# Kernel tuning notes

Measured on AMD Instinct MI355X. Metric: run time of the kernel, lower is better.

The kernel has to match this reference:

```python
import jax, jax.numpy as jnp
import numpy as np

TAU = 2.0          # LIF membrane time constant
V_TH = 1.0         # spike threshold (spikingjelly default)
BN_EPS = 1e-5

T, C_IN, C_OUT, L = 16, 512, 512, 4096


def setup_inputs() -> dict:
    key = jax.random.key(0)
    k1, k2 = jax.random.split(key)
    x = jax.random.normal(k1, (T, C_IN, L), dtype=jnp.float32)
    W = jax.random.normal(k2, (C_OUT, C_IN), dtype=jnp.float32) * 0.02
    gamma = jnp.ones((C_OUT,), dtype=jnp.float32)
    beta = jnp.zeros((C_OUT,), dtype=jnp.float32)
    return {"x": x, "W": W, "gamma": gamma, "beta": beta}


def reference(x, W, gamma, beta):
    # 1x1 Conv1d (bias=False): [T, Cin, L] x [Cout, Cin] -> [T, Cout, L]
    y = jnp.einsum("tcl,oc->tol", x, W)

    # BatchNorm1d in training mode: normalize per channel over (T, L)
    mean = jnp.mean(y, axis=(0, 2), keepdims=True)
    var = jnp.mean(jnp.square(y - mean), axis=(0, 2), keepdims=True)  # biased var
    y = (y - mean) * jax.lax.rsqrt(var + BN_EPS)
    y = y * gamma[None, :, None] + beta[None, :, None]

    # Multi-step LIF: v' = v + (x - v)/tau ; spike = H(v' - vth) ; hard reset to 0
    def step(v, x_t):
        v = v + (x_t - v) / TAU
        s = (v >= V_TH).astype(v.dtype)
        v = v * (1.0 - s)  # v_reset = 0
        return v, s

    v0 = jnp.zeros_like(y[0])
    _, spikes = jax.lax.scan(step, v0, y)
    return spikes
```

## Files before the change

### kernel.cpp

```cpp
#include <hip/hip_runtime.h>


#define T_STEPS 16
#define CIN 512
#define COUT 512
#define LDIM 4096
#define NL (COUT * LDIM)

static constexpr size_t NY = (size_t)T_STEPS * NL;

__device__ float g_yf[NY];
__device__ float g_wt[CIN * COUT];
__device__ float g_mr[2 * COUT];
__device__ int   g_bf16;

__device__ __forceinline__ float b2f(unsigned short u) {
    return __uint_as_float(((unsigned int)u) << 16);
}

__global__ void detect_dtype(const unsigned int* __restrict__ gamma_words) {
    if (threadIdx.x == 0)
        g_bf16 = (gamma_words[0] == 0x3F803F80u) ? 1 : 0;
}

__global__ __launch_bounds__(256) void wrepack(const void* __restrict__ win) {
    const int idx = blockIdx.x * 256 + threadIdx.x;
    const int k = idx >> 9;
    const int o = idx & 511;
    float v;
    if (g_bf16) v = b2f(((const unsigned short*)win)[(size_t)o * CIN + k]);
    else        v = ((const float*)win)[(size_t)o * CIN + k];
    g_wt[(size_t)k * COUT + o] = v;
}

__global__ __launch_bounds__(256) void gemm_sg(
    const void* __restrict__ xin, float* __restrict__ yws, int use_ws)
{
#pragma clang fp contract(off)
    float* __restrict__ y = use_ws ? yws : g_yf;
    const int bf = g_bf16;

    const int l  = blockIdx.x * 256 + threadIdx.x;
    const int og = blockIdx.y;
    const int t  = blockIdx.z;

    float acc[32];
    #pragma unroll
    for (int i = 0; i < 32; i++) acc[i] = 0.0f;

    const float* __restrict__ wt = g_wt + og * 32;

    if (bf) {
        const unsigned short* __restrict__ xp =
            (const unsigned short*)xin + (size_t)t * CIN * LDIM + l;
        #pragma unroll 2
        for (int k = 0; k < CIN; k++) {
            const float xv = b2f(xp[(size_t)k * LDIM]);
            const float* __restrict__ wr = wt + (size_t)k * COUT;
            #pragma unroll
            for (int i = 0; i < 32; i++)
                acc[i] = acc[i] + wr[i] * xv;
        }
    } else {
        const float* __restrict__ xp =
            (const float*)xin + (size_t)t * CIN * LDIM + l;
        #pragma unroll 2
        for (int k = 0; k < CIN; k++) {
            const float xv = xp[(size_t)k * LDIM];
            const float* __restrict__ wr = wt + (size_t)k * COUT;
            #pragma unroll
            for (int i = 0; i < 32; i++)
                acc[i] = acc[i] + wr[i] * xv;
        }
    }

    float* __restrict__ yp = y + ((size_t)t * COUT + og * 32) * LDIM + l;
    #pragma unroll
    for (int i = 0; i < 32; i++) yp[(size_t)i * LDIM] = acc[i];
}

__global__ __launch_bounds__(256) void bn_stats_np(
    const float* __restrict__ yws, int use_ws)
{
#pragma clang fp contract(off)
    const float* __restrict__ y = use_ws ? yws : g_yf;
    const int o = blockIdx.x;
    const int g = threadIdx.x >> 3;
    const int l = threadIdx.x & 7;

    __shared__ float leaves[32];
    __shared__ float mean_sh;
    __shared__ float acc_sh[2];

    for (int phase = 0; phase < 2; ++phase) {
        __syncthreads();
        const float mean = (phase == 1) ? mean_sh : 0.0f;
        for (int t = 0; t < T_STEPS; ++t) {
            const float* row = &y[(size_t)t * NL + (size_t)o * LDIM + g * 128];
            float r[8];
            #pragma unroll
            for (int q = 0; q < 8; q++) {
                float a = row[q * 8 + l];
                float b = row[64 + q * 8 + l];
                if (phase == 1) {
                    float da = a - mean; a = da * da;
                    float db = b - mean; b = db * db;
                }
                r[q] = a + b;
            }
            float s01 = r[0] + r[1], s23 = r[2] + r[3];
            float s45 = r[4] + r[5], s67 = r[6] + r[7];
            float S = (s01 + s23) + (s45 + s67);
            S = S + __shfl_xor(S, 1);
            S = S + __shfl_xor(S, 2);
            S = S + __shfl_xor(S, 4);
            __syncthreads();
            if (l == 0) leaves[g] = S;
            __syncthreads();
            if (threadIdx.x == 0) {
                float a16[16], a8[8], a4[4], a2[2];
                #pragma unroll
                for (int k = 0; k < 16; k++) a16[k] = leaves[2*k] + leaves[2*k+1];
                #pragma unroll
                for (int k = 0; k < 8;  k++) a8[k] = a16[2*k] + a16[2*k+1];
                #pragma unroll
                for (int k = 0; k < 4;  k++) a4[k] = a8[2*k] + a8[2*k+1];
                #pragma unroll
                for (int k = 0; k < 2;  k++) a2[k] = a4[2*k] + a4[2*k+1];
                float pw = a2[0] + a2[1];
                if (t == 0) acc_sh[phase] = pw;
                else        acc_sh[phase] = acc_sh[phase] + pw;
            }
            __syncthreads();
        }
        if (threadIdx.x == 0) {
            if (phase == 0) {
                mean_sh = __fdiv_rn(acc_sh[0], 65536.0f);
            } else {
                float var = __fdiv_rn(acc_sh[1], 65536.0f);
                float rr = __fdiv_rn(1.0f, __fsqrt_rn(var + 1e-5f));
                g_mr[o] = mean_sh;
                g_mr[COUT + o] = rr;
            }
        }
    }
}

__global__ __launch_bounds__(256) void lif_np(
    const void* __restrict__ gin, const void* __restrict__ bin,
    void* __restrict__ outv, const float* __restrict__ yws, int use_ws)
{
#pragma clang fp contract(off)
    const float* __restrict__ y = use_ws ? yws : g_yf;
    const int bf = g_bf16;
    const int idx = blockIdx.x * 256 + threadIdx.x;
    const int o = idx >> 12;
    const float mean = g_mr[o];
    const float r    = g_mr[COUT + o];
    float gm, bt;
    if (bf) {
        gm = b2f(((const unsigned short*)gin)[o]);
        bt = b2f(((const unsigned short*)bin)[o]);
    } else {
        gm = ((const float*)gin)[o];
        bt = ((const float*)bin)[o];
    }
    float v = 0.0f;
    #pragma unroll
    for (int t = 0; t < T_STEPS; t++) {
        float yv = y[(size_t)t * NL + idx];
        float d  = yv - mean;
        float n1 = d * r;
        float n2 = n1 * gm;
        float n3 = n2 + bt;
        float dv = n3 - v;
        float h  = dv * 0.5f;
        v = v + h;
        float s;
        if (v >= 1.0f) { s = 1.0f; v = 0.0f; } else { s = 0.0f; }
        if (bf) ((unsigned short*)outv)[(size_t)t * NL + idx] = (s == 1.0f) ? 0x3F80 : 0x0000;
        else    ((float*)outv)[(size_t)t * NL + idx] = s;
    }
}

extern "C" void kernel_launch(void* const* d_in, const int* in_sizes, int n_in,
                              void* d_out, int out_size, void* d_ws, size_t ws_size,
                              hipStream_t stream) {
    const void* x     = d_in[0];
    const void* W     = d_in[1];
    const void* gamma = d_in[2];
    const void* beta  = d_in[3];

    const int use_ws = (ws_size >= NY * sizeof(float)) ? 1 : 0;
    float* yws = (float*)d_ws;

    detect_dtype<<<1, 64, 0, stream>>>((const unsigned int*)gamma);

    wrepack<<<(CIN * COUT) / 256, 256, 0, stream>>>(W);

    dim3 grid(LDIM / 256, COUT / 32, T_STEPS);
    gemm_sg<<<grid, 256, 0, stream>>>(x, yws, use_ws);

    bn_stats_np<<<COUT, 256, 0, stream>>>(yws, use_ws);

    lif_np<<<NL / 256, 256, 0, stream>>>(gamma, beta, d_out, yws, use_ws);
}
```

Baseline: 812.1 us.

## Use packed FP32 mul/add with duplicated weights, two columns per thread

The GEMM now computes two adjacent L columns per thread, using v_pk_mul_f32 and v_pk_add_f32 inline asm. The weight repack stores each weight duplicated into a 64-bit pair so it can be a scalar operand. x loads and y stores become 2-wide vectors, and the grid halves along L. The goal is twice the FP32 throughput per instruction while keeping separate mul and add for bitwise matching. The trade-offs are doubled weight memory, more registers for the accumulators, and half as many threads.

```diff
diff --git a/kernel.cpp b/kernel.cpp
--- a/kernel.cpp
+++ b/kernel.cpp
@@ -6,11 +6,14 @@
 #define COUT 512
 #define LDIM 4096
 #define NL (COUT * LDIM)
+#define LP (LDIM / 2)
 
 static constexpr size_t NY = (size_t)T_STEPS * NL;
 
+typedef float v2f __attribute__((ext_vector_type(2)));
+
 __device__ float g_yf[NY];
-__device__ float g_wt[CIN * COUT];
+__device__ unsigned long long g_wt2[CIN * COUT];
 __device__ float g_mr[2 * COUT];
 __device__ int   g_bf16;
 
@@ -30,53 +33,68 @@
     float v;
     if (g_bf16) v = b2f(((const unsigned short*)win)[(size_t)o * CIN + k]);
     else        v = ((const float*)win)[(size_t)o * CIN + k];
-    g_wt[(size_t)k * COUT + o] = v;
-}
-
-__global__ __launch_bounds__(256) void gemm_sg(
+    const unsigned int b = __float_as_uint(v);
+    g_wt2[(size_t)k * COUT + o] = ((unsigned long long)b << 32) | b;
+}
+
+__global__ __launch_bounds__(256, 4) void gemm_pk(
     const void* __restrict__ xin, float* __restrict__ yws, int use_ws)
 {
 #pragma clang fp contract(off)
     float* __restrict__ y = use_ws ? yws : g_yf;
     const int bf = g_bf16;
 
-    const int l  = blockIdx.x * 256 + threadIdx.x;
+    const int lp = blockIdx.x * 256 + threadIdx.x;
     const int og = blockIdx.y;
     const int t  = blockIdx.z;
 
-    float acc[32];
+    v2f acc[32];
     #pragma unroll
-    for (int i = 0; i < 32; i++) acc[i] = 0.0f;
-
-    const float* __restrict__ wt = g_wt + og * 32;
+    for (int i = 0; i < 32; i++) { acc[i].x = 0.0f; acc[i].y = 0.0f; }
+
+    const unsigned long long* __restrict__ wt = g_wt2 + og * 32;
 
     if (bf) {
-        const unsigned short* __restrict__ xp =
-            (const unsigned short*)xin + (size_t)t * CIN * LDIM + l;
+        const unsigned int* __restrict__ xp =
+            (const unsigned int*)xin + (size_t)t * CIN * LP + lp;
         #pragma unroll 2
         for (int k = 0; k < CIN; k++) {
-            const float xv = b2f(xp[(size_t)k * LDIM]);
-            const float* __restrict__ wr = wt + (size_t)k * COUT;
+            const unsigned int u = xp[(size_t)k * LP];
+            v2f x2;
+            x2.x = __uint_as_float(u << 16);
+            x2.y = __uint_as_float(u & 0xffff0000u);
+            const unsigned long long* __restrict__ wr = wt + (size_t)k * COUT;
             #pragma unroll
-            for (int i = 0; i < 32; i++)
-                acc[i] = acc[i] + wr[i] * xv;
+            for (int i = 0; i < 32; i++) {
+                v2f p;
+                asm("v_pk_mul_f32 %0, %1, %2"
+                    : "=v"(p) : "s"(wr[i]), "v"(x2));
+                asm("v_pk_add_f32 %0, %1, %2"
+                    : "=v"(acc[i]) : "v"(acc[i]), "v"(p));
+            }
         }
     } else {
-        const float* __restrict__ xp =
-            (const float*)xin + (size_t)t * CIN * LDIM + l;
+        const v2f* __restrict__ xp =
+            (const v2f*)xin + (size_t)t * CIN * LP + lp;
         #pragma unroll 2
         for (int k = 0; k < CIN; k++) {
-            const float xv = xp[(size_t)k * LDIM];
-            const float* __restrict__ wr = wt + (size_t)k * COUT;
+            v2f x2 = xp[(size_t)k * LP];
+            const unsigned long long* __restrict__ wr = wt + (size_t)k * COUT;
             #pragma unroll
-            for (int i = 0; i < 32; i++)
-                acc[i] = acc[i] + wr[i] * xv;
-        }
-    }
-
-    float* __restrict__ yp = y + ((size_t)t * COUT + og * 32) * LDIM + l;
+            for (int i = 0; i < 32; i++) {
+                v2f p;
+                asm("v_pk_mul_f32 %0, %1, %2"
+                    : "=v"(p) : "s"(wr[i]), "v"(x2));
+                asm("v_pk_add_f32 %0, %1, %2"
+                    : "=v"(acc[i]) : "v"(acc[i]), "v"(p));
+            }
+        }
+    }
+
+    float* __restrict__ yp = y + ((size_t)t * COUT + og * 32) * LDIM + 2 * lp;
     #pragma unroll
-    for (int i = 0; i < 32; i++) yp[(size_t)i * LDIM] = acc[i];
+    for (int i = 0; i < 32; i++)
+        *(v2f*)(yp + (size_t)i * LDIM) = acc[i];
 }
 
 __global__ __launch_bounds__(256) void bn_stats_np(
@@ -198,8 +216,8 @@
 
     wrepack<<<(CIN * COUT) / 256, 256, 0, stream>>>(W);
 
-    dim3 grid(LDIM / 256, COUT / 32, T_STEPS);
-    gemm_sg<<<grid, 256, 0, stream>>>(x, yws, use_ws);
+    dim3 grid(LDIM / 512, COUT / 32, T_STEPS);
+    gemm_pk<<<grid, 256, 0, stream>>>(x, yws, use_ws);
 
     bn_stats_np<<<COUT, 256, 0, stream>>>(yws, use_ws);
 
```

Result: slower. 829.6 us (+2.2%).

## Rewrite conv GEMM in inline assembly with packed FP32 math and scalar weight loads

Applied to the files above, without the earlier changes.

Replaces the compiler-generated SIMT GEMM with a hand-written assembly loop. Each thread now handles two adjacent L positions, using v_pk_mul/v_pk_add on duplicated weight pairs. The 32 weights per k step are loaded into scalar registers with s_load_dwordx16 instead of per-lane vector loads. A separate pre-pass converts bf16 input to an fp32 buffer so the asm path only handles fp32. The aim is to halve the VALU instruction count and cut redundant weight loads. The cost is a full wait on every k iteration with no prefetch, an extra global fp32 buffer, and fragile hard-coded register clobbers.

```diff
diff --git a/kernel.cpp b/kernel.cpp
--- a/kernel.cpp
+++ b/kernel.cpp
@@ -6,11 +6,14 @@
 #define COUT 512
 #define LDIM 4096
 #define NL (COUT * LDIM)
+#define LP (LDIM / 2)
 
 static constexpr size_t NY = (size_t)T_STEPS * NL;
+static constexpr size_t NX = (size_t)T_STEPS * CIN * LDIM;
 
 __device__ float g_yf[NY];
-__device__ float g_wt[CIN * COUT];
+__device__ float g_xf[NX];
+__device__ unsigned long long g_wt2[CIN * COUT];
 __device__ float g_mr[2 * COUT];
 __device__ int   g_bf16;
 
@@ -30,53 +33,137 @@
     float v;
     if (g_bf16) v = b2f(((const unsigned short*)win)[(size_t)o * CIN + k]);
     else        v = ((const float*)win)[(size_t)o * CIN + k];
-    g_wt[(size_t)k * COUT + o] = v;
-}
-
-__global__ __launch_bounds__(256) void gemm_sg(
+    const unsigned int b = __float_as_uint(v);
+    g_wt2[(size_t)k * COUT + o] = ((unsigned long long)b << 32) | b;
+}
+
+__global__ __launch_bounds__(256) void xconv(const void* __restrict__ xin) {
+    if (!g_bf16) return;
+    const size_t e = ((size_t)blockIdx.x * 256 + threadIdx.x) * 8;
+    const uint4 u = *(const uint4*)((const unsigned short*)xin + e);
+    float4 f0, f1;
+    f0.x = __uint_as_float(u.x << 16);
+    f0.y = __uint_as_float(u.x & 0xffff0000u);
+    f0.z = __uint_as_float(u.y << 16);
+    f0.w = __uint_as_float(u.y & 0xffff0000u);
+    f1.x = __uint_as_float(u.z << 16);
+    f1.y = __uint_as_float(u.z & 0xffff0000u);
+    f1.z = __uint_as_float(u.w << 16);
+    f1.w = __uint_as_float(u.w & 0xffff0000u);
+    float4* out = (float4*)(g_xf + e);
+    out[0] = f0;
+    out[1] = f1;
+}
+
+
+#define VZ(N) "v_mov_b32 v" #N ", 0\n\t"
+
+#define PKQ(R0, R1)                                              \
+    "v_pk_mul_f32 v[98:99], s[" R0 "], v[96:97]\n\t"             \
+    "v_pk_mul_f32 v[100:101], s[" R1 "], v[96:97]\n\t"           \
+    "v_pk_add_f32 v[" R0 "], v[" R0 "], v[98:99]\n\t"            \
+    "v_pk_add_f32 v[" R1 "], v[" R1 "], v[100:101]\n\t"
+
+#define STQ(R)                                                   \
+    "global_store_dwordx2 %[XOFF], v[" R "], s[28:29]\n\t"       \
+    "s_add_u32 s28, s28, 16384\n\t"                              \
+    "s_addc_u32 s29, s29, 0\n\t"
+
+__global__ __launch_bounds__(256) void gemm_asm(
     const void* __restrict__ xin, float* __restrict__ yws, int use_ws)
 {
-#pragma clang fp contract(off)
-    float* __restrict__ y = use_ws ? yws : g_yf;
+    float* y = use_ws ? yws : g_yf;
     const int bf = g_bf16;
 
-    const int l  = blockIdx.x * 256 + threadIdx.x;
+    const int lp = blockIdx.x * 256 + threadIdx.x;
     const int og = blockIdx.y;
     const int t  = blockIdx.z;
 
-    float acc[32];
-    #pragma unroll
-    for (int i = 0; i < 32; i++) acc[i] = 0.0f;
-
-    const float* __restrict__ wt = g_wt + og * 32;
-
-    if (bf) {
-        const unsigned short* __restrict__ xp =
-            (const unsigned short*)xin + (size_t)t * CIN * LDIM + l;
-        #pragma unroll 2
-        for (int k = 0; k < CIN; k++) {
-            const float xv = b2f(xp[(size_t)k * LDIM]);
-            const float* __restrict__ wr = wt + (size_t)k * COUT;
-            #pragma unroll
-            for (int i = 0; i < 32; i++)
-                acc[i] = acc[i] + wr[i] * xv;
-        }
-    } else {
-        const float* __restrict__ xp =
-            (const float*)xin + (size_t)t * CIN * LDIM + l;
-        #pragma unroll 2
-        for (int k = 0; k < CIN; k++) {
-            const float xv = xp[(size_t)k * LDIM];
-            const float* __restrict__ wr = wt + (size_t)k * COUT;
-            #pragma unroll
-            for (int i = 0; i < 32; i++)
-                acc[i] = acc[i] + wr[i] * xv;
-        }
-    }
-
-    float* __restrict__ yp = y + ((size_t)t * COUT + og * 32) * LDIM + l;
-    #pragma unroll
-    for (int i = 0; i < 32; i++) yp[(size_t)i * LDIM] = acc[i];
+    const float* xsel = bf ? g_xf : (const float*)xin;
+
+    const unsigned long long xb =
+        (unsigned long long)(uintptr_t)xsel +
+        (unsigned long long)t * CIN * LDIM * 4ull;
+    const unsigned long long wb =
+        (unsigned long long)(uintptr_t)g_wt2 + (unsigned long long)og * 256ull;
+    const unsigned long long yb =
+        (unsigned long long)(uintptr_t)y +
+        (((unsigned long long)t * COUT + (unsigned long long)og * 32) * LDIM) * 4ull;
+    const unsigned int xoffb = (unsigned int)lp * 8u;
+
+    asm volatile(
+        "s_mov_b64 s[28:29], %[WB]\n\t"
+        "s_mov_b64 s[30:31], %[XB]\n\t"
+        "s_mov_b32 s26, 512\n\t"
+        VZ(32) VZ(33) VZ(34) VZ(35) VZ(36) VZ(37) VZ(38) VZ(39)
+        VZ(40) VZ(41) VZ(42) VZ(43) VZ(44) VZ(45) VZ(46) VZ(47)
+        VZ(48) VZ(49) VZ(50) VZ(51) VZ(52) VZ(53) VZ(54) VZ(55)
+        VZ(56) VZ(57) VZ(58) VZ(59) VZ(60) VZ(61) VZ(62) VZ(63)
+        VZ(64) VZ(65) VZ(66) VZ(67) VZ(68) VZ(69) VZ(70) VZ(71)
+        VZ(72) VZ(73) VZ(74) VZ(75) VZ(76) VZ(77) VZ(78) VZ(79)
+        VZ(80) VZ(81) VZ(82) VZ(83) VZ(84) VZ(85) VZ(86) VZ(87)
+        VZ(88) VZ(89) VZ(90) VZ(91) VZ(92) VZ(93) VZ(94) VZ(95)
+        "Lg%=:\n\t"
+        "s_load_dwordx16 s[32:47], s[28:29], 0x0\n\t"
+        "s_load_dwordx16 s[48:63], s[28:29], 0x40\n\t"
+        "s_load_dwordx16 s[64:79], s[28:29], 0x80\n\t"
+        "s_load_dwordx16 s[80:95], s[28:29], 0xc0\n\t"
+        "global_load_dwordx2 v[96:97], %[XOFF], s[30:31]\n\t"
+        "s_add_u32 s28, s28, 4096\n\t"
+        "s_addc_u32 s29, s29, 0\n\t"
+        "s_add_u32 s30, s30, 16384\n\t"
+        "s_addc_u32 s31, s31, 0\n\t"
+        "s_waitcnt vmcnt(0) lgkmcnt(0)\n\t"
+        PKQ("32:33", "34:35")
+        PKQ("36:37", "38:39")
+        PKQ("40:41", "42:43")
+        PKQ("44:45", "46:47")
+        PKQ("48:49", "50:51")
+        PKQ("52:53", "54:55")
+        PKQ("56:57", "58:59")
+        PKQ("60:61", "62:63")
+        PKQ("64:65", "66:67")
+        PKQ("68:69", "70:71")
+        PKQ("72:73", "74:75")
+        PKQ("76:77", "78:79")
+        PKQ("80:81", "82:83")
+        PKQ("84:85", "86:87")
+        PKQ("88:89", "90:91")
+        PKQ("92:93", "94:95")
+        "s_sub_u32 s26, s26, 1\n\t"
+        "s_cmp_lg_u32 s26, 0\n\t"
+        "s_cbranch_scc1 Lg%=\n\t"
+        "s_mov_b64 s[28:29], %[YB]\n\t"
+        STQ("32:33") STQ("34:35") STQ("36:37") STQ("38:39")
+        STQ("40:41") STQ("42:43") STQ("44:45") STQ("46:47")
+        STQ("48:49") STQ("50:51") STQ("52:53") STQ("54:55")
+        STQ("56:57") STQ("58:59") STQ("60:61") STQ("62:63")
+        STQ("64:65") STQ("66:67") STQ("68:69") STQ("70:71")
+        STQ("72:73") STQ("74:75") STQ("76:77") STQ("78:79")
+        STQ("80:81") STQ("82:83") STQ("84:85") STQ("86:87")
+        STQ("88:89") STQ("90:91") STQ("92:93") STQ("94:95")
+        "s_waitcnt vmcnt(0)\n\t"
+        :
+        : [WB] "s"(wb), [XB] "s"(xb), [YB] "s"(yb), [XOFF] "v"(xoffb)
+        : "memory", "scc",
+          "s26", "s28", "s29", "s30", "s31",
+          "s32", "s33", "s34", "s35", "s36", "s37", "s38", "s39",
+          "s40", "s41", "s42", "s43", "s44", "s45", "s46", "s47",
+          "s48", "s49", "s50", "s51", "s52", "s53", "s54", "s55",
+          "s56", "s57", "s58", "s59", "s60", "s61", "s62", "s63",
+          "s64", "s65", "s66", "s67", "s68", "s69", "s70", "s71",
+          "s72", "s73", "s74", "s75", "s76", "s77", "s78", "s79",
+          "s80", "s81", "s82", "s83", "s84", "s85", "s86", "s87",
+          "s88", "s89", "s90", "s91", "s92", "s93", "s94", "s95",
+          "v32", "v33", "v34", "v35", "v36", "v37", "v38", "v39",
+          "v40", "v41", "v42", "v43", "v44", "v45", "v46", "v47",
+          "v48", "v49", "v50", "v51", "v52", "v53", "v54", "v55",
+          "v56", "v57", "v58", "v59", "v60", "v61", "v62", "v63",
+          "v64", "v65", "v66", "v67", "v68", "v69", "v70", "v71",
+          "v72", "v73", "v74", "v75", "v76", "v77", "v78", "v79",
+          "v80", "v81", "v82", "v83", "v84", "v85", "v86", "v87",
+          "v88", "v89", "v90", "v91", "v92", "v93", "v94", "v95",
+          "v96", "v97", "v98", "v99", "v100", "v101");
 }
 
 __global__ __launch_bounds__(256) void bn_stats_np(
@@ -198,8 +285,10 @@
 
     wrepack<<<(CIN * COUT) / 256, 256, 0, stream>>>(W);
 
-    dim3 grid(LDIM / 256, COUT / 32, T_STEPS);
-    gemm_sg<<<grid, 256, 0, stream>>>(x, yws, use_ws);
+    xconv<<<(int)(NX / (256 * 8)), 256, 0, stream>>>(x);
+
+    dim3 grid(LDIM / 512, COUT / 32, T_STEPS);
+    gemm_asm<<<grid, 256, 0, stream>>>(x, yws, use_ws);
 
     bn_stats_np<<<COUT, 256, 0, stream>>>(yws, use_ws);
 
```

New measurement: 933.1 us. +14.9%, slower.

## Stage GEMM weight tiles in double-buffered LDS instead of global reads

Applied to the files above, without the earlier changes.

The 1x1-conv GEMM kernel now loads 64x32 weight tiles into shared memory with a two-stage double buffer, prefetching the next tile into registers while computing on the current one. This replaces per-k uniform global/scalar-cache weight reads with LDS broadcast reads. It also adds an occupancy hint of 6 blocks per SM via launch bounds. The cost is extra barriers, plus LDS read instructions and VGPR pressure for the weights.

```diff
diff --git a/kernel.cpp b/kernel.cpp
--- a/kernel.cpp
+++ b/kernel.cpp
@@ -33,44 +33,93 @@
     g_wt[(size_t)k * COUT + o] = v;
 }
 
-__global__ __launch_bounds__(256) void gemm_sg(
+__global__ __launch_bounds__(256, 6) void gemm_lds(
     const void* __restrict__ xin, float* __restrict__ yws, int use_ws)
 {
 #pragma clang fp contract(off)
     float* __restrict__ y = use_ws ? yws : g_yf;
     const int bf = g_bf16;
 
-    const int l  = blockIdx.x * 256 + threadIdx.x;
+    const int tid = threadIdx.x;
+    const int l  = blockIdx.x * 256 + tid;
     const int og = blockIdx.y;
     const int t  = blockIdx.z;
+
+    __shared__ float wlds[2][64][32];
+
+    const int row  = tid >> 2;
+    const int part = tid & 3;
+    const float* __restrict__ wsrc =
+        g_wt + (size_t)row * COUT + og * 32 + part * 8;
+
+    {
+        const float4* s4 = (const float4*)wsrc;
+        float4 r0 = s4[0], r1 = s4[1];
+        float4* d4 = (float4*)&wlds[0][row][part * 8];
+        d4[0] = r0;
+        d4[1] = r1;
+    }
+    __syncthreads();
 
     float acc[32];
     #pragma unroll
     for (int i = 0; i < 32; i++) acc[i] = 0.0f;
 
-    const float* __restrict__ wt = g_wt + og * 32;
-
     if (bf) {
         const unsigned short* __restrict__ xp =
             (const unsigned short*)xin + (size_t)t * CIN * LDIM + l;
-        #pragma unroll 2
-        for (int k = 0; k < CIN; k++) {
-            const float xv = b2f(xp[(size_t)k * LDIM]);
-            const float* __restrict__ wr = wt + (size_t)k * COUT;
-            #pragma unroll
-            for (int i = 0; i < 32; i++)
-                acc[i] = acc[i] + wr[i] * xv;
+        for (int c = 0; c < 8; ++c) {
+            float4 r0, r1;
+            if (c < 7) {
+                const float4* s4 =
+                    (const float4*)(wsrc + (size_t)(c + 1) * 64 * COUT);
+                r0 = s4[0];
+                r1 = s4[1];
+            }
+            const float (* __restrict__ wb)[32] = wlds[c & 1];
+            const unsigned short* __restrict__ xc = xp + (size_t)c * 64 * LDIM;
+            #pragma unroll 8
+            for (int kk = 0; kk < 64; ++kk) {
+                const float xv = b2f(xc[(size_t)kk * LDIM]);
+                const float* __restrict__ wr = wb[kk];
+                #pragma unroll
+                for (int i = 0; i < 32; i++)
+                    acc[i] = acc[i] + wr[i] * xv;
+            }
+            if (c < 7) {
+                float4* d4 = (float4*)&wlds[(c & 1) ^ 1][row][part * 8];
+                d4[0] = r0;
+                d4[1] = r1;
+            }
+            __syncthreads();
         }
     } else {
         const float* __restrict__ xp =
             (const float*)xin + (size_t)t * CIN * LDIM + l;
-        #pragma unroll 2
-        for (int k = 0; k < CIN; k++) {
-            const float xv = xp[(size_t)k * LDIM];
-            const float* __restrict__ wr = wt + (size_t)k * COUT;
-            #pragma unroll
-            for (int i = 0; i < 32; i++)
-                acc[i] = acc[i] + wr[i] * xv;
+        for (int c = 0; c < 8; ++c) {
+            float4 r0, r1;
+            if (c < 7) {
+                const float4* s4 =
+                    (const float4*)(wsrc + (size_t)(c + 1) * 64 * COUT);
+                r0 = s4[0];
+                r1 = s4[1];
+            }
+            const float (* __restrict__ wb)[32] = wlds[c & 1];
+            const float* __restrict__ xc = xp + (size_t)c * 64 * LDIM;
+            #pragma unroll 8
+            for (int kk = 0; kk < 64; ++kk) {
+                const float xv = xc[(size_t)kk * LDIM];
+                const float* __restrict__ wr = wb[kk];
+                #pragma unroll
+                for (int i = 0; i < 32; i++)
+                    acc[i] = acc[i] + wr[i] * xv;
+            }
+            if (c < 7) {
+                float4* d4 = (float4*)&wlds[(c & 1) ^ 1][row][part * 8];
+                d4[0] = r0;
+                d4[1] = r1;
+            }
+            __syncthreads();
         }
     }
 
@@ -199,7 +248,7 @@
     wrepack<<<(CIN * COUT) / 256, 256, 0, stream>>>(W);
 
     dim3 grid(LDIM / 256, COUT / 32, T_STEPS);
-    gemm_sg<<<grid, 256, 0, stream>>>(x, yws, use_ws);
+    gemm_lds<<<grid, 256, 0, stream>>>(x, yws, use_ws);
 
     bn_stats_np<<<COUT, 256, 0, stream>>>(yws, use_ws);
 
```

Result: slower. 1.245 ms (+53.3%).
